# Optimization experiments

Measured on AMD Instinct MI355X. Metric: run time of the kernel, lower is better.

## Reference

```python
import jax, jax.numpy as jnp
import numpy as np

N = 524288   # tokens (accounts)
D = 9        # num_prop_size
E = 2        # expert_size
H = 128      # expert MLP hidden
M = 32       # moe_out
O = 2        # output_size
K = 1        # top-k
LOSS_COF = 0.01
EPS = 1e-10


def setup_inputs() -> dict:
    key = jax.random.key(0)
    ks = jax.random.split(key, 10)
    f32 = jnp.float32
    return {
        "num_prop": jax.random.normal(ks[0], (N, D), f32),
        "cat_prop": jax.random.normal(ks[1], (N, 3), f32),
        "w_gate": jax.random.normal(ks[2], (D, E), f32) * 0.1,
        "W1": jax.random.normal(ks[3], (E, D, H), f32) * 0.1,
        "b1": jax.random.normal(ks[4], (E, H), f32) * 0.01,
        "W2": jax.random.normal(ks[5], (E, H, M), f32) * 0.1,
        "b2": jax.random.normal(ks[6], (E, M), f32) * 0.01,
        "Wout": jax.random.normal(ks[7], (M, O), f32) * 0.1,
        "bout": jax.random.normal(ks[8], (O,), f32) * 0.01,
        "k": K,
    }


def _cv_squared(x):
    # torch: x.var() (unbiased) / (x.mean()**2 + eps)
    return jnp.var(x, ddof=1) / (jnp.mean(x) ** 2 + EPS)


def reference(num_prop, cat_prop, w_gate, W1, b1, W2, b2, Wout, bout, k):
    x = num_prop                                   # eval mode: dropout = identity
    n, e = x.shape[0], w_gate.shape[1]

    # --- top-k gating (eval: clean logits, no noise) ---
    logits = x @ w_gate                            # [N, E]
    top_logits, top_idx = jax.lax.top_k(logits, min(k + 1, e))
    top_k_gates = jax.nn.softmax(top_logits[:, :k], axis=1)   # [N, k]
    rows = jnp.arange(n)[:, None]
    gates = jnp.zeros_like(logits).at[rows, top_idx[:, :k]].set(top_k_gates)  # [N, E]

    importance = gates.sum(axis=0)                 # [E]
    load = (gates > 0).astype(jnp.float32).sum(axis=0)  # [E]
    loss = (_cv_squared(importance) + _cv_squared(load)) * LOSS_COF

    # --- experts: per-expert 2-layer MLP, computed dense (E=2) then gated combine ---
    h = jax.nn.relu(jnp.einsum("nd,edh->neh", x, W1) + b1)    # [N, E, H]
    y_e = jnp.einsum("neh,ehm->nem", h, W2) + b2              # [N, E, M]
    y = jnp.einsum("ne,nem->nm", gates, y_e)                  # [N, M]

    out = y @ Wout + bout                                     # [N, O]
    return (out, loss)
```

## Files before the change

kernel.cpp:

```cpp
#include <hip/hip_runtime.h>

#define NTOK 524288
#define TPB  256
#define TOKB 512
#define NBLK (NTOK / TOKB)

__device__ __forceinline__ float bf2f(unsigned short u) {
    union { unsigned int i; float f; } v;
    v.i = ((unsigned int)u) << 16;
    return v.f;
}

__device__ __forceinline__ float ldq(const void* p, int i, bool f32) {
    if (f32) return ((const float*)p)[i];
    return bf2f(((const unsigned short*)p)[i]);
}

__global__ void prep_kernel(const void* __restrict__ num_prop,
                            const void* __restrict__ wgate,
                            const void* __restrict__ W1,
                            const void* __restrict__ b1,
                            const void* __restrict__ W2,
                            const void* __restrict__ b2,
                            const void* __restrict__ Wout,
                            const void* __restrict__ bout,
                            unsigned int* __restrict__ cnt1,
                            int* __restrict__ flag,
                            float* __restrict__ bpp,
                            float* __restrict__ wgf,
                            float* __restrict__ wpack)
{
    __shared__ unsigned int bad;
    __shared__ int sflag;
    const int t = threadIdx.x;
    if (t == 0) { bad = 0u; *cnt1 = 0u; }
    __syncthreads();
    if (t < 72) {
        const unsigned short* u = (const unsigned short*)num_prop;
        int e = (u[t] >> 7) & 0xFF;
        if (e < 64 || e > 191) atomicOr(&bad, 1u);
    }
    __syncthreads();
    if (t == 0) { sflag = (int)bad; *flag = (int)bad; }
    __syncthreads();
    const bool f32 = (sflag != 0);

    if (t < 18) wgf[t] = ldq(wgate, t, f32);

    if (t < 4) {
        int e = t >> 1, o = t & 1;
        float acc = ldq(bout, o, f32);
        for (int m = 0; m < 32; ++m)
            acc += ldq(b2, e * 32 + m, f32) * ldq(Wout, m * 2 + o, f32);
        bpp[t] = acc;
    }

    const int e = t >> 7;
    const int j = t & 127;
    float p0 = 0.f, p1 = 0.f;
    for (int m = 0; m < 32; ++m) {
        float w = ldq(W2, (e * 128 + j) * 32 + m, f32);
        p0 += w * ldq(Wout, m * 2 + 0, f32);
        p1 += w * ldq(Wout, m * 2 + 1, f32);
    }
    float* dst = wpack + e * 1536 + j * 12;
    #pragma unroll
    for (int d = 0; d < 9; ++d)
        dst[d] = ldq(W1, (e * 9 + d) * 128 + j, f32);
    dst[9]  = ldq(b1, e * 128 + j, f32);
    dst[10] = p0;
    dst[11] = p1;
}

__global__ __launch_bounds__(TPB, 5)
void moe_main(const void* __restrict__ xg,
              const int* __restrict__ flag,
              const float* __restrict__ wgf,
              const float* __restrict__ bpp,
              const float* __restrict__ wpack,
              unsigned int* __restrict__ cnt1,
              float2* __restrict__ out)
{
    __shared__ __align__(16) float xs[TOKB * 9];
    __shared__ __align__(16) float wsm[3072];
    __shared__ unsigned short smap[TOKB];
    __shared__ unsigned int wcnt[8];

    const int tid  = threadIdx.x;
    const int lane = tid & 63;
    const int wave = tid >> 6;

    const bool f32 = (*flag) != 0;
    const int gbase = blockIdx.x * (TOKB * 9);

    #pragma unroll
    for (int i = 0; i < 12; ++i)
        wsm[tid + i * TPB] = wpack[tid + i * TPB];

    if (f32) {
        const float* xf = (const float*)xg;
        #pragma unroll
        for (int i = 0; i < 18; ++i)
            xs[tid + i * TPB] = xf[gbase + tid + i * TPB];
    } else {
        const unsigned short* xu = (const unsigned short*)xg;
        for (int i = tid; i < TOKB * 9; i += TPB)
            xs[i] = bf2f(xu[gbase + i]);
    }
    __syncthreads();

    float l0A = 0.f, l1A = 0.f, l0B = 0.f, l1B = 0.f;
    #pragma unroll
    for (int d = 0; d < 9; ++d) {
        const float wa = wgf[d * 2 + 0], wb = wgf[d * 2 + 1];
        const float xA = xs[tid * 9 + d];
        const float xB = xs[(tid + 256) * 9 + d];
        l0A = fmaf(xA, wa, l0A); l1A = fmaf(xA, wb, l1A);
        l0B = fmaf(xB, wa, l0B); l1B = fmaf(xB, wb, l1B);
    }
    const bool e1A = l1A > l0A;
    const bool e1B = l1B > l0B;

    unsigned long long balA = __ballot(e1A);
    unsigned long long balB = __ballot(e1B);
    if (lane == 0) {
        wcnt[wave]     = (unsigned int)__popcll(balA);
        wcnt[4 + wave] = (unsigned int)__popcll(balB);
    }
    __syncthreads();
    int pres[8]; int run = 0;
    #pragma unroll
    for (int c = 0; c < 8; ++c) { pres[c] = run; run += (int)wcnt[c]; }
    const int n1 = run;
    const int n0 = TOKB - n1;
    const unsigned long long below = (1ull << lane) - 1ull;
    const int prA = pres[wave]     + (int)__popcll(balA & below);
    const int prB = pres[4 + wave] + (int)__popcll(balB & below);
    const int slotA = e1A ? (n0 + prA) : (tid - prA);
    const int slotB = e1B ? (n0 + prB) : (tid + 256 - prB);
    smap[slotA] = (unsigned short)tid;
    smap[slotB] = (unsigned short)(tid + 256);
    __syncthreads();

    const int sA = tid * 2, sB = sA + 1;
    const int tA = (int)smap[sA], tB = (int)smap[sB];
    float xa[9], xb[9];
    #pragma unroll
    for (int d = 0; d < 9; ++d) { xa[d] = xs[tA * 9 + d]; xb[d] = xs[tB * 9 + d]; }

    const int wbase = __builtin_amdgcn_readfirstlane(tid & 192) << 1;
    const int n0u   = __builtin_amdgcn_readfirstlane(n0);

    float2 ra, rb;
    if (n0u <= wbase || n0u >= wbase + 128) {
        const int ew = (n0u <= wbase) ? 1 : 0;
        const float* wp = wsm + ew * 1536;
        float a0 = bpp[ew * 2 + 0], a1 = bpp[ew * 2 + 1];
        float c0 = a0, c1 = a1;
        #pragma unroll 2
        for (int j = 0; j < 128; ++j) {
            const float* r = wp + j * 12;
            float hA = r[9], hB = r[9];
            #pragma unroll
            for (int d = 0; d < 9; ++d) {
                hA = fmaf(xa[d], r[d], hA);
                hB = fmaf(xb[d], r[d], hB);
            }
            hA = fmaxf(hA, 0.f); hB = fmaxf(hB, 0.f);
            a0 = fmaf(hA, r[10], a0); a1 = fmaf(hA, r[11], a1);
            c0 = fmaf(hB, r[10], c0); c1 = fmaf(hB, r[11], c1);
        }
        ra.x = a0; ra.y = a1; rb.x = c0; rb.y = c1;
    } else {
        const bool eA = (sA >= n0u), eB = (sB >= n0u);
        float aA0 = bpp[0], aA1 = bpp[1], aA2 = bpp[2], aA3 = bpp[3];
        float aB0 = bpp[0], aB1 = bpp[1], aB2 = bpp[2], aB3 = bpp[3];
        #pragma unroll 2
        for (int j = 0; j < 128; ++j) {
            const float* r0 = wsm + j * 12;
            const float* r1 = wsm + 1536 + j * 12;
            float hA0 = r0[9], hA1 = r1[9], hB0 = r0[9], hB1 = r1[9];
            #pragma unroll
            for (int d = 0; d < 9; ++d) {
                hA0 = fmaf(xa[d], r0[d], hA0);
                hA1 = fmaf(xa[d], r1[d], hA1);
                hB0 = fmaf(xb[d], r0[d], hB0);
                hB1 = fmaf(xb[d], r1[d], hB1);
            }
            hA0 = fmaxf(hA0, 0.f); hA1 = fmaxf(hA1, 0.f);
            hB0 = fmaxf(hB0, 0.f); hB1 = fmaxf(hB1, 0.f);
            aA0 = fmaf(hA0, r0[10], aA0); aA1 = fmaf(hA0, r0[11], aA1);
            aA2 = fmaf(hA1, r1[10], aA2); aA3 = fmaf(hA1, r1[11], aA3);
            aB0 = fmaf(hB0, r0[10], aB0); aB1 = fmaf(hB0, r0[11], aB1);
            aB2 = fmaf(hB1, r1[10], aB2); aB3 = fmaf(hB1, r1[11], aB3);
        }
        ra.x = eA ? aA2 : aA0; ra.y = eA ? aA3 : aA1;
        rb.x = eB ? aB2 : aB0; rb.y = eB ? aB3 : aB1;
    }

    __syncthreads();
    float2* ob = (float2*)xs;
    ob[tA] = ra;
    ob[tB] = rb;
    __syncthreads();
    const int obase = blockIdx.x * TOKB;
    out[obase + tid]       = ob[tid];
    out[obase + 256 + tid] = ob[256 + tid];
    if (tid == 0) atomicAdd(cnt1, (unsigned int)n1);
}

__global__ void finalize_kernel(const unsigned int* __restrict__ cnt1,
                                float* __restrict__ loss_out)
{
    double c1 = (double)(*cnt1);
    double c0 = (double)NTOK - c1;
    double diff = c0 - c1;
    double mean = (double)NTOK * 0.5;
    double var  = 0.5 * diff * diff;
    double cv2  = var / (mean * mean + 1e-10);
    *loss_out = (float)(0.02 * cv2);
}

extern "C" void kernel_launch(void* const* d_in, const int* in_sizes, int n_in,
                              void* d_out, int out_size, void* d_ws, size_t ws_size,
                              hipStream_t stream) {
    const void* num_prop = d_in[0];
    const void* w_gate   = d_in[2];
    const void* W1       = d_in[3];
    const void* b1       = d_in[4];
    const void* W2       = d_in[5];
    const void* b2       = d_in[6];
    const void* Wout     = d_in[7];
    const void* bout     = d_in[8];

    char* ws = (char*)d_ws;
    unsigned int* cnt1 = (unsigned int*)ws;
    int* flag          = (int*)(ws + 8);
    float* bpp         = (float*)(ws + 16);
    float* wgf         = (float*)(ws + 64);
    float* wpack       = (float*)(ws + 192);

    float*  outf = (float*)d_out;
    float2* out2 = (float2*)d_out;

    hipLaunchKernelGGL(prep_kernel, dim3(1), dim3(256), 0, stream,
                       num_prop, w_gate, W1, b1, W2, b2, Wout, bout,
                       cnt1, flag, bpp, wgf, wpack);
    hipLaunchKernelGGL(moe_main, dim3(NBLK), dim3(TPB), 0, stream,
                       num_prop, flag, wgf, bpp, wpack, cnt1, out2);
    hipLaunchKernelGGL(finalize_kernel, dim3(1), dim3(1), 0, stream,
                       cnt1, outf + (size_t)NTOK * 2);
}
```

Measured before the change: 127.8 us.

## Process eight tokens per thread with per-thread expert choice and straddle fixup

Each block now handles 2048 tokens, and each thread computes 8 sorted tokens. One weight row loaded from shared memory is reused across those 8 tokens, and the next row is software-prefetched as float4 values. The per-wave mixed-expert path is replaced by a single expert per thread; threads whose 8 slots cross the expert boundary get a correction pass that recomputes the expert-1 tokens. Input loads become float4. Fewer, larger blocks with launch bounds of 1 and more registers per thread may reduce occupancy and the number of blocks available to fill the CUs.

After: 139.9 us. +9.4%, slower.

```diff
diff --git a/kernel.cpp b/kernel.cpp
--- a/kernel.cpp
+++ b/kernel.cpp
@@ -2,7 +2,7 @@
 
 #define NTOK 524288
 #define TPB  256
-#define TOKB 512
+#define TOKB 2048
 #define NBLK (NTOK / TOKB)
 
 __device__ __forceinline__ float bf2f(unsigned short u) {
@@ -72,7 +72,7 @@
     dst[11] = p1;
 }
 
-__global__ __launch_bounds__(TPB, 5)
+__global__ __launch_bounds__(TPB, 1)
 void moe_main(const void* __restrict__ xg,
               const int* __restrict__ flag,
               const float* __restrict__ wgf,
@@ -84,129 +84,139 @@
     __shared__ __align__(16) float xs[TOKB * 9];
     __shared__ __align__(16) float wsm[3072];
     __shared__ unsigned short smap[TOKB];
-    __shared__ unsigned int wcnt[8];
+    __shared__ unsigned int wcnt[32];
 
     const int tid  = threadIdx.x;
     const int lane = tid & 63;
     const int wave = tid >> 6;
 
     const bool f32 = (*flag) != 0;
-    const int gbase = blockIdx.x * (TOKB * 9);
 
     #pragma unroll
     for (int i = 0; i < 12; ++i)
         wsm[tid + i * TPB] = wpack[tid + i * TPB];
 
     if (f32) {
-        const float* xf = (const float*)xg;
+        const float4* xf4 = (const float4*)xg;
+        float4* xsv = (float4*)xs;
+        const int g4 = blockIdx.x * (TOKB * 9 / 4);
         #pragma unroll
         for (int i = 0; i < 18; ++i)
-            xs[tid + i * TPB] = xf[gbase + tid + i * TPB];
+            xsv[tid + i * TPB] = xf4[g4 + tid + i * TPB];
     } else {
         const unsigned short* xu = (const unsigned short*)xg;
+        const int gbase = blockIdx.x * (TOKB * 9);
         for (int i = tid; i < TOKB * 9; i += TPB)
             xs[i] = bf2f(xu[gbase + i]);
     }
     __syncthreads();
 
-    float l0A = 0.f, l1A = 0.f, l0B = 0.f, l1B = 0.f;
-    #pragma unroll
-    for (int d = 0; d < 9; ++d) {
-        const float wa = wgf[d * 2 + 0], wb = wgf[d * 2 + 1];
-        const float xA = xs[tid * 9 + d];
-        const float xB = xs[(tid + 256) * 9 + d];
-        l0A = fmaf(xA, wa, l0A); l1A = fmaf(xA, wb, l1A);
-        l0B = fmaf(xB, wa, l0B); l1B = fmaf(xB, wb, l1B);
-    }
-    const bool e1A = l1A > l0A;
-    const bool e1B = l1B > l0B;
-
-    unsigned long long balA = __ballot(e1A);
-    unsigned long long balB = __ballot(e1B);
-    if (lane == 0) {
-        wcnt[wave]     = (unsigned int)__popcll(balA);
-        wcnt[4 + wave] = (unsigned int)__popcll(balB);
-    }
-    __syncthreads();
-    int pres[8]; int run = 0;
-    #pragma unroll
-    for (int c = 0; c < 8; ++c) { pres[c] = run; run += (int)wcnt[c]; }
+    bool e1g[8];
+    unsigned long long balg[8];
+    #pragma unroll
+    for (int g = 0; g < 8; ++g) {
+        float l0 = 0.f, l1 = 0.f;
+        #pragma unroll
+        for (int d = 0; d < 9; ++d) {
+            float xv = xs[(g * 256 + tid) * 9 + d];
+            l0 = fmaf(xv, wgf[d * 2 + 0], l0);
+            l1 = fmaf(xv, wgf[d * 2 + 1], l1);
+        }
+        e1g[g] = l1 > l0;
+        balg[g] = __ballot(e1g[g]);
+        if (lane == 0) wcnt[g * 4 + wave] = (unsigned int)__popcll(balg[g]);
+    }
+    __syncthreads();
+
+    int pres[32]; int run = 0;
+    #pragma unroll
+    for (int c = 0; c < 32; ++c) { pres[c] = run; run += (int)wcnt[c]; }
     const int n1 = run;
     const int n0 = TOKB - n1;
     const unsigned long long below = (1ull << lane) - 1ull;
-    const int prA = pres[wave]     + (int)__popcll(balA & below);
-    const int prB = pres[4 + wave] + (int)__popcll(balB & below);
-    const int slotA = e1A ? (n0 + prA) : (tid - prA);
-    const int slotB = e1B ? (n0 + prB) : (tid + 256 - prB);
-    smap[slotA] = (unsigned short)tid;
-    smap[slotB] = (unsigned short)(tid + 256);
-    __syncthreads();
-
-    const int sA = tid * 2, sB = sA + 1;
-    const int tA = (int)smap[sA], tB = (int)smap[sB];
-    float xa[9], xb[9];
-    #pragma unroll
-    for (int d = 0; d < 9; ++d) { xa[d] = xs[tA * 9 + d]; xb[d] = xs[tB * 9 + d]; }
-
-    const int wbase = __builtin_amdgcn_readfirstlane(tid & 192) << 1;
-    const int n0u   = __builtin_amdgcn_readfirstlane(n0);
-
-    float2 ra, rb;
-    if (n0u <= wbase || n0u >= wbase + 128) {
-        const int ew = (n0u <= wbase) ? 1 : 0;
-        const float* wp = wsm + ew * 1536;
-        float a0 = bpp[ew * 2 + 0], a1 = bpp[ew * 2 + 1];
-        float c0 = a0, c1 = a1;
-        #pragma unroll 2
+    #pragma unroll
+    for (int g = 0; g < 8; ++g) {
+        const int tok = g * 256 + tid;
+        const int pr  = pres[g * 4 + wave] + (int)__popcll(balg[g] & below);
+        const int slot = e1g[g] ? (n0 + pr) : (tok - pr);
+        smap[slot] = (unsigned short)tok;
+    }
+    if (tid == 0) atomicAdd(cnt1, (unsigned int)n1);
+    __syncthreads();
+
+    const int s0 = tid * 8;
+    int tkv[8];
+    #pragma unroll
+    for (int k = 0; k < 8; ++k) tkv[k] = (int)smap[s0 + k];
+    float x[8][9];
+    #pragma unroll
+    for (int k = 0; k < 8; ++k)
+        #pragma unroll
+        for (int d = 0; d < 9; ++d) x[k][d] = xs[tkv[k] * 9 + d];
+
+    const int ex = (s0 >= n0) ? 1 : 0;
+    const float* wp = wsm + ex * 1536;
+    float a0[8], a1[8];
+    #pragma unroll
+    for (int k = 0; k < 8; ++k) { a0[k] = bpp[ex * 2 + 0]; a1[k] = bpp[ex * 2 + 1]; }
+
+    const float4* q0 = (const float4*)wp;
+    float4 A = q0[0], B = q0[1], C = q0[2];
+    for (int j = 0; j < 128; ++j) {
+        const int jn = (j + 1) & 127;
+        const float4* qn = (const float4*)(wp + jn * 12);
+        const float4 An = qn[0], Bn = qn[1], Cn = qn[2];
+        #pragma unroll
+        for (int k = 0; k < 8; ++k) {
+            float h = C.y;
+            h = fmaf(x[k][0], A.x, h); h = fmaf(x[k][1], A.y, h);
+            h = fmaf(x[k][2], A.z, h); h = fmaf(x[k][3], A.w, h);
+            h = fmaf(x[k][4], B.x, h); h = fmaf(x[k][5], B.y, h);
+            h = fmaf(x[k][6], B.z, h); h = fmaf(x[k][7], B.w, h);
+            h = fmaf(x[k][8], C.x, h);
+            h = fmaxf(h, 0.f);
+            a0[k] = fmaf(h, C.z, a0[k]);
+            a1[k] = fmaf(h, C.w, a1[k]);
+        }
+        A = An; B = Bn; C = Cn;
+    }
+
+    const int nw = (n0 & 7) ? (8 - (n0 & 7)) : 0;
+    float fx0 = 0.f, fx1 = 0.f; int ftk = 0;
+    if (tid < nw) {
+        ftk = (int)smap[n0 + tid];
+        float xr[9];
+        #pragma unroll
+        for (int d = 0; d < 9; ++d) xr[d] = xs[ftk * 9 + d];
+        fx0 = bpp[2]; fx1 = bpp[3];
+        const float* wq = wsm + 1536;
         for (int j = 0; j < 128; ++j) {
-            const float* r = wp + j * 12;
-            float hA = r[9], hB = r[9];
-            #pragma unroll
-            for (int d = 0; d < 9; ++d) {
-                hA = fmaf(xa[d], r[d], hA);
-                hB = fmaf(xb[d], r[d], hB);
-            }
-            hA = fmaxf(hA, 0.f); hB = fmaxf(hB, 0.f);
-            a0 = fmaf(hA, r[10], a0); a1 = fmaf(hA, r[11], a1);
-            c0 = fmaf(hB, r[10], c0); c1 = fmaf(hB, r[11], c1);
+            const float4* q = (const float4*)(wq + j * 12);
+            const float4 Af = q[0], Bf = q[1], Cf = q[2];
+            float h = Cf.y;
+            h = fmaf(xr[0], Af.x, h); h = fmaf(xr[1], Af.y, h);
+            h = fmaf(xr[2], Af.z, h); h = fmaf(xr[3], Af.w, h);
+            h = fmaf(xr[4], Bf.x, h); h = fmaf(xr[5], Bf.y, h);
+            h = fmaf(xr[6], Bf.z, h); h = fmaf(xr[7], Bf.w, h);
+            h = fmaf(xr[8], Cf.x, h);
+            h = fmaxf(h, 0.f);
+            fx0 = fmaf(h, Cf.z, fx0);
+            fx1 = fmaf(h, Cf.w, fx1);
         }
-        ra.x = a0; ra.y = a1; rb.x = c0; rb.y = c1;
-    } else {
-        const bool eA = (sA >= n0u), eB = (sB >= n0u);
-        float aA0 = bpp[0], aA1 = bpp[1], aA2 = bpp[2], aA3 = bpp[3];
-        float aB0 = bpp[0], aB1 = bpp[1], aB2 = bpp[2], aB3 = bpp[3];
-        #pragma unroll 2
-        for (int j = 0; j < 128; ++j) {
-            const float* r0 = wsm + j * 12;
-            const float* r1 = wsm + 1536 + j * 12;
-            float hA0 = r0[9], hA1 = r1[9], hB0 = r0[9], hB1 = r1[9];
-            #pragma unroll
-            for (int d = 0; d < 9; ++d) {
-                hA0 = fmaf(xa[d], r0[d], hA0);
-                hA1 = fmaf(xa[d], r1[d], hA1);
-                hB0 = fmaf(xb[d], r0[d], hB0);
-                hB1 = fmaf(xb[d], r1[d], hB1);
-            }
-            hA0 = fmaxf(hA0, 0.f); hA1 = fmaxf(hA1, 0.f);
-            hB0 = fmaxf(hB0, 0.f); hB1 = fmaxf(hB1, 0.f);
-            aA0 = fmaf(hA0, r0[10], aA0); aA1 = fmaf(hA0, r0[11], aA1);
-            aA2 = fmaf(hA1, r1[10], aA2); aA3 = fmaf(hA1, r1[11], aA3);
-            aB0 = fmaf(hB0, r0[10], aB0); aB1 = fmaf(hB0, r0[11], aB1);
-            aB2 = fmaf(hB1, r1[10], aB2); aB3 = fmaf(hB1, r1[11], aB3);
-        }
-        ra.x = eA ? aA2 : aA0; ra.y = eA ? aA3 : aA1;
-        rb.x = eB ? aB2 : aB0; rb.y = eB ? aB3 : aB1;
     }
 
     __syncthreads();
     float2* ob = (float2*)xs;
-    ob[tA] = ra;
-    ob[tB] = rb;
+    #pragma unroll
+    for (int k = 0; k < 8; ++k)
+        ob[tkv[k]] = make_float2(a0[k], a1[k]);
+    __syncthreads();
+    if (tid < nw) ob[ftk] = make_float2(fx0, fx1);
     __syncthreads();
     const int obase = blockIdx.x * TOKB;
-    out[obase + tid]       = ob[tid];
-    out[obase + 256 + tid] = ob[256 + tid];
-    if (tid == 0) atomicAdd(cnt1, (unsigned int)n1);
+    #pragma unroll
+    for (int g = 0; g < 8; ++g)
+        out[obase + g * 256 + tid] = ob[g * 256 + tid];
 }
 
 __global__ void finalize_kernel(const unsigned int* __restrict__ cnt1,
```
